# Kernel tuning notes

Measured on AMD Instinct MI355X. Metric: run time of the kernel, lower is better.

The kernel has to match this reference:

```python
import jax, jax.numpy as jnp
import numpy as np

S = 4        # support_num
NEI = 32     # neighbor_num for conv stages
POOL_NEI = 4 # neighbor_num inside Pool_layer
EPS = 1e-12


def sq_dist(a, b):
    # a: (b,m,3), b: (b,n,3) -> (b,m,n)
    return (jnp.sum(a * a, -1)[:, :, None] + jnp.sum(b * b, -1)[:, None, :]
            - 2.0 * jnp.einsum('bmd,bnd->bmn', a, b))


def query_ball(radius, k, points, queries):
    # PointNet++-style ball query: up to k indices within radius, padded with first hit.
    d = sq_dist(queries, points)                      # (b,m,n)
    n = points.shape[1]
    idx = jnp.broadcast_to(jnp.arange(n, dtype=jnp.int32), d.shape)
    idx = jnp.where(d > radius * radius, n, idx)
    idx = jnp.sort(idx, axis=-1)[..., :k]             # (b,m,k)
    first = idx[..., :1]
    return jnp.where(idx == n, first, idx)


def gather_nb(feat, idx):
    # feat: (b,v,c), idx: (b,v,k) -> (b,v,k,c)
    return jax.vmap(lambda f, i: f[i])(feat, idx)


def neighbor_dir_norm(verts, idx):
    nb = gather_nb(verts, idx)                        # (b,v,k,3)
    d = nb - verts[:, :, None, :]
    return d / (jnp.linalg.norm(d, axis=-1, keepdims=True) + EPS)


def conv_surface(idx, verts, dirs):
    # dirs: (3, S*out). Geometric-only first layer of 3DGCN.
    b, v, k = idx.shape
    o = dirs.shape[1] // S
    dn = neighbor_dir_norm(verts, idx)                # (b,v,k,3)
    sd = dirs / (jnp.linalg.norm(dirs, axis=0, keepdims=True) + EPS)
    theta = jnp.maximum(jnp.einsum('bvkd,dm->bvkm', dn, sd), 0.0)
    theta = theta.reshape(b, v, k, S, o)
    return theta.max(axis=2).sum(axis=2)              # (b,v,o)


def conv_layer(idx, verts, feat, w, bias, dirs):
    # w: (cin,(S+1)*o), bias: ((S+1)*o,), dirs: (3,S*o)
    b, v, k = idx.shape
    o = dirs.shape[1] // S
    dn = neighbor_dir_norm(verts, idx)
    sd = dirs / (jnp.linalg.norm(dirs, axis=0, keepdims=True) + EPS)
    theta = jnp.maximum(jnp.einsum('bvkd,dm->bvkm', dn, sd), 0.0)  # (b,v,k,S*o)
    fout = feat @ w + bias                            # (b,v,(S+1)*o)
    center, supp = fout[..., :o], fout[..., o:]
    supp_nb = gather_nb(supp, idx)                    # (b,v,k,S*o)
    act = (theta * supp_nb).reshape(b, v, k, S, o).max(axis=2).sum(axis=2)
    return center + act


def pool(verts, feat, radius):
    idx = query_ball(radius, POOL_NEI, verts, verts)
    pooled = gather_nb(feat, idx).max(axis=2)         # (b,v,c)
    m = verts.shape[1] // 2                           # pooling_rate = 2 (deterministic subsample)
    return verts[:, :m], pooled[:, :m]


def setup_inputs() -> dict:
    key = jax.random.key(0)
    ks = jax.random.split(key, 32)
    B, V = 4, 4096
    inp = {}
    inp['vertices'] = jax.random.uniform(ks[0], (B, V, 3), dtype=jnp.float32)
    inp['surf_dirs'] = jax.random.normal(ks[1], (3, S * 32), dtype=jnp.float32) * 0.1
    specs = [(1, 32, 32), (3, 64, 32), (4, 96, 32), (6, 128, 32), (7, 160, 32),
             (8, 192, 32), (9, 224, 32), (10, 256, 32), (11, 288, 1024)]
    i = 2
    for n, cin, cout in specs:
        inp[f'w{n}'] = jax.random.normal(ks[i], (cin, (S + 1) * cout), dtype=jnp.float32) / np.sqrt(cin); i += 1
        inp[f'b{n}'] = jnp.zeros(((S + 1) * cout,), jnp.float32)
        inp[f'd{n}'] = jax.random.normal(ks[i], (3, S * cout), dtype=jnp.float32) * 0.1; i += 1
    inp['fc1_w'] = jax.random.normal(ks[i], (1024, 256), dtype=jnp.float32) * 0.03; i += 1
    inp['fc1_b'] = jnp.zeros((256,), jnp.float32)
    inp['bn_g'] = jnp.ones((256,), jnp.float32)
    inp['bn_b'] = jnp.zeros((256,), jnp.float32)
    inp['bn_m'] = jnp.zeros((256,), jnp.float32)
    inp['bn_v'] = jnp.ones((256,), jnp.float32)
    inp['fc2_w'] = jax.random.normal(ks[i], (256, 40), dtype=jnp.float32) * 0.06
    inp['fc2_b'] = jnp.zeros((40,), jnp.float32)
    return inp


def reference(vertices, surf_dirs, w1, b1, d1, w3, b3, d3, w4, b4, d4, w6, b6, d6,
              w7, b7, d7, w8, b8, d8, w9, b9, d9, w10, b10, d10, w11, b11, d11,
              fc1_w, fc1_b, bn_g, bn_b, bn_m, bn_v, fc2_w, fc2_b):
    relu = lambda x: jnp.maximum(x, 0.0)
    verts = vertices
    idx = query_ball(0.2, NEI, verts, verts)
    fm0 = relu(conv_surface(idx, verts, surf_dirs))
    fm1 = relu(conv_layer(idx, verts, fm0, w1, b1, d1))
    fm1 = jnp.concatenate([fm0, fm1], -1)
    verts, fm1 = pool(verts, fm1, 0.2)
    idx = query_ball(0.4, NEI, verts, verts)
    fm3 = relu(conv_layer(idx, verts, fm1, w3, b3, d3)); fm3 = jnp.concatenate([fm1, fm3], -1)
    fm4 = relu(conv_layer(idx, verts, fm3, w4, b4, d4)); fm4 = jnp.concatenate([fm3, fm4], -1)
    verts, fm4 = pool(verts, fm4, 0.4)
    idx = query_ball(0.6, NEI, verts, verts)
    fm6 = relu(conv_layer(idx, verts, fm4, w6, b6, d6)); fm6 = jnp.concatenate([fm4, fm6], -1)
    fm7 = relu(conv_layer(idx, verts, fm6, w7, b7, d7)); fm7 = jnp.concatenate([fm6, fm7], -1)
    verts, fm7 = pool(verts, fm7, 0.6)
    idx = query_ball(0.8, NEI, verts, verts)
    fm8 = relu(conv_layer(idx, verts, fm7, w8, b8, d8)); fm8 = jnp.concatenate([fm7, fm8], -1)
    fm9 = relu(conv_layer(idx, verts, fm8, w9, b9, d9)); fm9 = jnp.concatenate([fm8, fm9], -1)
    verts, fm9 = pool(verts, fm9, 0.8)
    idx = query_ball(1.0, NEI, verts, verts)
    fm10 = relu(conv_layer(idx, verts, fm9, w10, b10, d10)); fm10 = jnp.concatenate([fm9, fm10], -1)
    fm11 = conv_layer(idx, verts, fm10, w11, b11, d11)
    g = fm11.max(axis=1)                              # (b,1024) global max pool
    h = g @ fc1_w + fc1_b                             # Dropout is identity at inference
    h = (h - bn_m) / jnp.sqrt(bn_v + 1e-5) * bn_g + bn_b
    h = relu(h)
    return h @ fc2_w + fc2_b                          # (b,40)
```

## Files before the change

kernel.cpp:

```cpp
#include <hip/hip_runtime.h>
#include <hip/hip_bf16.h>
#include <math.h>

#define DEV __device__ __forceinline__

DEV float frn_mul(float a, float b) { return __fmul_rn(a, b); }
DEV float frn_add(float a, float b) { return __fadd_rn(a, b); }

union BFU { __hip_bfloat16 h; unsigned short u; };

typedef __attribute__((ext_vector_type(8))) short short8v;
typedef __attribute__((ext_vector_type(4))) float f32x4;

__global__ void pack4_kernel(const float* __restrict__ v, float4* __restrict__ out,
                             int n)
{
    int t = blockIdx.x * blockDim.x + threadIdx.x;
    if (t >= n) return;
    float x = v[(size_t)t * 3 + 0], y = v[(size_t)t * 3 + 1], z = v[(size_t)t * 3 + 2];
    float pn = frn_add(frn_add(frn_mul(x, x), frn_mul(y, y)), frn_mul(z, z));
    out[t] = make_float4(x, y, z, pn);
}

DEV void qb_scan2(const float4* __restrict__ pts, int V, float4 q4, float r2,
                  int lane, int* __restrict__ row)
{
    float qx = q4.x, qy = q4.y, qz = q4.z, qn = q4.w;
    int count = 0;
    int first = -1;
    float4 pbuf[2];
#pragma unroll
    for (int u = 0; u < 2; ++u) pbuf[u] = pts[u * 64 + lane];
    for (int base = 0; base < V && count < 32; base += 128) {
#pragma unroll
        for (int u = 0; u < 2; ++u) {
            float4 p = pbuf[u];
            pbuf[u] = pts[base + 128 + u * 64 + lane];
            float dt = frn_add(frn_add(frn_mul(qx, p.x), frn_mul(qy, p.y)), frn_mul(qz, p.z));
            float d = __fsub_rn(frn_add(qn, p.w), frn_mul(2.0f, dt));
            bool in = !(d > r2);
            unsigned long long mask = __ballot(in);
            if (first < 0 && mask != 0ull)
                first = base + u * 64 + (int)__ffsll((long long)mask) - 1;
            int pos = count + (int)__popcll(mask & ((1ull << lane) - 1ull));
            if (in && pos < 32) row[pos] = base + u * 64 + lane;
            count += (int)__popcll(mask);
        }
    }
    int cnt = count < 32 ? count : 32;
    for (int t = cnt + lane; t < 32; t += 64) row[t] = first;
}

__global__ __launch_bounds__(256)
void mega_start_kernel(const float4* __restrict__ vp1,
                       const float* __restrict__ dirs,
                       float* __restrict__ outF, int Cw,
                       int* __restrict__ idx1, int* __restrict__ idx2,
                       int* __restrict__ idx3, int* __restrict__ idx4,
                       int* __restrict__ idx5,
                       const float* __restrict__ w11, unsigned short* __restrict__ wt)
{
    __shared__ int rowS[4][32];
    int bid = blockIdx.x;
    int tid = threadIdx.x;
    int lane = tid & 63;

    if (bid < 4096) {
        int wid = (bid * 256 + tid) >> 6;
        int wql = tid >> 6;
        int b = wid >> 12;
        float4 q4 = vp1[(size_t)wid];
        float qx = q4.x, qy = q4.y, qz = q4.z, qn = q4.w;
        const float4* pts = vp1 + (size_t)b * 4096;
        int* row = idx1 + (size_t)wid * 32;

        int count = 0;
        int first = -1;
        float4 pbuf[4];
#pragma unroll
        for (int u = 0; u < 4; ++u) pbuf[u] = pts[u * 64 + lane];
        for (int base = 0; base < 4096 && count < 32; base += 256) {
#pragma unroll
            for (int u = 0; u < 4; ++u) {
                float4 p = pbuf[u];
                pbuf[u] = pts[base + 256 + u * 64 + lane];
                float dt = frn_add(frn_add(frn_mul(qx, p.x), frn_mul(qy, p.y)), frn_mul(qz, p.z));
                float d = __fsub_rn(frn_add(qn, p.w), frn_mul(2.0f, dt));
                bool in = !(d > 0.04f);
                unsigned long long mask = __ballot(in);
                if (first < 0 && mask != 0ull)
                    first = base + u * 64 + (int)__ffsll((long long)mask) - 1;
                int pos = count + (int)__popcll(mask & ((1ull << lane) - 1ull));
                if (in && pos < 32) { row[pos] = base + u * 64 + lane; rowS[wql][pos] = base + u * 64 + lane; }
                count += (int)__popcll(mask);
            }
        }
        int cnt = count < 32 ? count : 32;
        for (int t = cnt + lane; t < 32; t += 64) { row[t] = first; rowS[wql][t] = first; }
        __syncthreads();

        float dnx, dny, dnz;
        {
            int k = lane & 31;
            float4 nb4 = pts[rowS[wql][k]];
            float dx = nb4.x - qx;
            float dy = nb4.y - qy;
            float dz = nb4.z - qz;
            float nrm = sqrtf(dx * dx + dy * dy + dz * dz) + 1e-12f;
            float inv = 1.0f / nrm;
            dnx = dx * inv; dny = dy * inv; dnz = dz * inv;
        }
        int m1 = lane, m2 = lane + 64;
        float ax = dirs[m1], ay = dirs[128 + m1], az = dirs[256 + m1];
        float i1 = 1.0f / (sqrtf(ax * ax + ay * ay + az * az) + 1e-12f);
        ax *= i1; ay *= i1; az *= i1;
        float bx = dirs[m2], by = dirs[128 + m2], bz = dirs[256 + m2];
        float i2 = 1.0f / (sqrtf(bx * bx + by * by + bz * bz) + 1e-12f);
        bx *= i2; by *= i2; bz *= i2;

        float mx1 = -INFINITY, mx2 = -INFINITY;
        for (int k = 0; k < 32; ++k) {
            float ex = __shfl(dnx, k, 64);
            float ey = __shfl(dny, k, 64);
            float ez = __shfl(dnz, k, 64);
            float t1 = fmaxf(ex * ax + ey * ay + ez * az, 0.0f);
            float t2 = fmaxf(ex * bx + ey * by + ez * bz, 0.0f);
            mx1 = fmaxf(mx1, t1);
            mx2 = fmaxf(mx2, t2);
        }
        float part = mx1 + mx2;
        float tot = part + __shfl_xor(part, 32, 64);
        if (lane < 32) {
            outF[(size_t)wid * Cw + lane] = fmaxf(tot, 0.0f);
        }
    } else if (bid < 7936) {
        int V, r_bid; float r2; int* idxp;
        if (bid < 6144)      { V = 2048; r2 = 0.16f; idxp = idx2; r_bid = bid - 4096; }
        else if (bid < 7168) { V = 1024; r2 = 0.36f; idxp = idx3; r_bid = bid - 6144; }
        else if (bid < 7680) { V = 512;  r2 = 0.64f; idxp = idx4; r_bid = bid - 7168; }
        else                 { V = 256;  r2 = 1.0f;  idxp = idx5; r_bid = bid - 7680; }
        int widl = (r_bid * 256 + tid) >> 6;
        int b = widl / V;
        int v = widl - b * V;
        float4 q4 = vp1[(size_t)b * 4096 + v];
        const float4* pts = vp1 + (size_t)b * 4096;
        qb_scan2(pts, V, q4, r2, lane, idxp + (size_t)widl * 32);
    } else {
        int t = (bid - 7936) * 256 + tid;
        if (t < 5120 * 36) {
            int kc = t / 5120;
            int n = t - kc * 5120;
            BFU a;
            ushort4 o0, o1;
            a.h = __float2bfloat16(w11[(size_t)(kc * 8 + 0) * 5120 + n]); o0.x = a.u;
            a.h = __float2bfloat16(w11[(size_t)(kc * 8 + 1) * 5120 + n]); o0.y = a.u;
            a.h = __float2bfloat16(w11[(size_t)(kc * 8 + 2) * 5120 + n]); o0.z = a.u;
            a.h = __float2bfloat16(w11[(size_t)(kc * 8 + 3) * 5120 + n]); o0.w = a.u;
            a.h = __float2bfloat16(w11[(size_t)(kc * 8 + 4) * 5120 + n]); o1.x = a.u;
            a.h = __float2bfloat16(w11[(size_t)(kc * 8 + 5) * 5120 + n]); o1.y = a.u;
            a.h = __float2bfloat16(w11[(size_t)(kc * 8 + 6) * 5120 + n]); o1.z = a.u;
            a.h = __float2bfloat16(w11[(size_t)(kc * 8 + 7) * 5120 + n]); o1.w = a.u;
            *(ushort4*)&wt[(size_t)n * 288 + kc * 8] = o0;
            *(ushort4*)&wt[(size_t)n * 288 + kc * 8 + 4] = o1;
        }
    }
}

__global__ __launch_bounds__(256)
void gemm_tiled_kernel(const float* __restrict__ feat, int Cw, int cin,
                       const float* __restrict__ w, const float* __restrict__ bias,
                       int N, float* __restrict__ fout)
{
    __shared__ float As[64][36];
    __shared__ float Bs[32][68];

    int m0 = blockIdx.x * 64;
    int n0 = blockIdx.y * 64;
    int tid = threadIdx.x;
    int tx = tid & 15, ty = tid >> 4;

    float acc[4][4];
#pragma unroll
    for (int i = 0; i < 4; ++i)
#pragma unroll
        for (int j = 0; j < 4; ++j) acc[i][j] = 0.0f;

    for (int k0 = 0; k0 < cin; k0 += 32) {
#pragma unroll
        for (int i = 0; i < 2; ++i) {
            int qq = tid + i * 256;
            int row = qq >> 3, c = qq & 7;
            float4 v = *(const float4*)&feat[(size_t)(m0 + row) * Cw + k0 + 4 * c];
            *(float4*)&As[row][4 * c] = v;
        }
#pragma unroll
        for (int i = 0; i < 2; ++i) {
            int qq = tid + i * 256;
            int kr = qq >> 4, c = qq & 15;
            int n = n0 + 4 * c;
            float4 v = make_float4(0.0f, 0.0f, 0.0f, 0.0f);
            if (n < N) v = *(const float4*)&w[(size_t)(k0 + kr) * N + n];
            *(float4*)&Bs[kr][4 * c] = v;
        }
        __syncthreads();

#pragma unroll
        for (int kt = 0; kt < 32; kt += 4) {
            float4 av4[4], bv4[4];
#pragma unroll
            for (int i = 0; i < 4; ++i) av4[i] = *(const float4*)&As[ty * 4 + i][kt];
#pragma unroll
            for (int r = 0; r < 4; ++r) bv4[r] = *(const float4*)&Bs[kt + r][tx * 4];
            const float* a = (const float*)av4;
            const float* bb = (const float*)bv4;
#pragma unroll
            for (int i = 0; i < 4; ++i)
#pragma unroll
                for (int r = 0; r < 4; ++r)
#pragma unroll
                    for (int j = 0; j < 4; ++j)
                        acc[i][j] = fmaf(a[i * 4 + r], bb[r * 4 + j], acc[i][j]);
        }
        __syncthreads();
    }

    int n = n0 + tx * 4;
    if (n < N) {
        float b0 = bias[n + 0], b1 = bias[n + 1], b2 = bias[n + 2], b3 = bias[n + 3];
#pragma unroll
        for (int i = 0; i < 4; ++i) {
            int m = m0 + ty * 4 + i;
            float4 o;
            o.x = acc[i][0] + b0;
            o.y = acc[i][1] + b1;
            o.z = acc[i][2] + b2;
            o.w = acc[i][3] + b3;
            *(float4*)&fout[(size_t)m * N + n] = o;
        }
    }
}

__global__ __launch_bounds__(256)
void gemm_mfma_conv11(const unsigned short* __restrict__ Abf,
                      const unsigned short* __restrict__ WTbf,
                      const float* __restrict__ bias,
                      __hip_bfloat16* __restrict__ fout)
{
    __shared__ unsigned short As[128][40];
    __shared__ unsigned short Bs[128][40];
    const int K = 288, N = 5120;
    int m0 = blockIdx.x * 128;
    int n0 = blockIdx.y * 128;
    int tid = threadIdx.x;
    int lane = tid & 63;
    int wave = tid >> 6;
    int wm = wave & 1, wn = wave >> 1;
    int l15 = lane & 15, l4 = lane >> 4;

    f32x4 acc[4][4];
#pragma unroll
    for (int mi = 0; mi < 4; ++mi)
#pragma unroll
        for (int ni = 0; ni < 4; ++ni) acc[mi][ni] = (f32x4){0.f, 0.f, 0.f, 0.f};

    for (int k0 = 0; k0 < K; k0 += 32) {
#pragma unroll
        for (int i = 0; i < 2; ++i) {
            int c = tid + i * 256;
            int row = c >> 2, qq = c & 3;
            *(uint4*)&As[row][qq * 8] = *(const uint4*)&Abf[(size_t)(m0 + row) * K + k0 + qq * 8];
            *(uint4*)&Bs[row][qq * 8] = *(const uint4*)&WTbf[(size_t)(n0 + row) * K + k0 + qq * 8];
        }
        __syncthreads();

        short8v af[4], bfv[4];
#pragma unroll
        for (int mi = 0; mi < 4; ++mi)
            af[mi] = *(const short8v*)&As[wm * 64 + mi * 16 + l15][l4 * 8];
#pragma unroll
        for (int ni = 0; ni < 4; ++ni)
            bfv[ni] = *(const short8v*)&Bs[wn * 64 + ni * 16 + l15][l4 * 8];
#pragma unroll
        for (int mi = 0; mi < 4; ++mi)
#pragma unroll
            for (int ni = 0; ni < 4; ++ni)
                acc[mi][ni] = __builtin_amdgcn_mfma_f32_16x16x32_bf16(af[mi], bfv[ni], acc[mi][ni], 0, 0, 0);
        __syncthreads();
    }

#pragma unroll
    for (int ni = 0; ni < 4; ++ni) {
        int col = n0 + wn * 64 + ni * 16 + l15;
        float bv = bias[col];
#pragma unroll
        for (int mi = 0; mi < 4; ++mi) {
            int rbase = m0 + wm * 64 + mi * 16 + l4 * 4;
#pragma unroll
            for (int j = 0; j < 4; ++j) {
                BFU u;
                u.h = __float2bfloat16(acc[mi][ni][j] + bv);
                *(unsigned short*)&fout[(size_t)(rbase + j) * N + col] = u.u;
            }
        }
    }
}

__global__ void conv_agg32_kernel(const int* __restrict__ idx,
                                  const float4* __restrict__ vp1,
                                  const float* __restrict__ fout,
                                  const float* __restrict__ dirs,
                                  float* __restrict__ outF, int Cw, int coff,
                                  int V, int do_relu,
                                  unsigned short* __restrict__ abf)
{
    int blk = blockIdx.x;
    int b = (blk & 7) >> 1;
    int j = ((blk >> 3) << 1) | (blk & 1);
    int vloc = j * 4 + (int)(threadIdx.x >> 6);
    int wid = b * V + vloc;
    int lane = threadIdx.x & 63;

    float dnx, dny, dnz;
    int nbrow;
    {
        int k = lane & 31;
        int nb = idx[(size_t)wid * 32 + k];
        nbrow = b * V + nb;
        float4 c4 = vp1[(size_t)b * 4096 + vloc];
        float4 n4 = vp1[(size_t)b * 4096 + nb];
        float dx = n4.x - c4.x;
        float dy = n4.y - c4.y;
        float dz = n4.z - c4.z;
        float nrm = sqrtf(dx * dx + dy * dy + dz * dz) + 1e-12f;
        float inv = 1.0f / nrm;
        dnx = dx * inv; dny = dy * inv; dnz = dz * inv;
    }
    int m1 = lane, m2 = lane + 64;
    float ax = dirs[m1], ay = dirs[128 + m1], az = dirs[256 + m1];
    float i1 = 1.0f / (sqrtf(ax * ax + ay * ay + az * az) + 1e-12f);
    ax *= i1; ay *= i1; az *= i1;
    float bx = dirs[m2], by = dirs[128 + m2], bz = dirs[256 + m2];
    float i2 = 1.0f / (sqrtf(bx * bx + by * by + bz * bz) + 1e-12f);
    bx *= i2; by *= i2; bz *= i2;

    float a1[4] = {-INFINITY, -INFINITY, -INFINITY, -INFINITY};
    float a2[4] = {-INFINITY, -INFINITY, -INFINITY, -INFINITY};
#pragma unroll
    for (int kk = 0; kk < 32; kk += 4) {
#pragma unroll
        for (int u = 0; u < 4; ++u) {
            int k = kk + u;
            float ex = __shfl(dnx, k, 64);
            float ey = __shfl(dny, k, 64);
            float ez = __shfl(dnz, k, 64);
            int nr = __shfl(nbrow, k, 64);
            const float* fr = fout + (size_t)nr * 160 + 32;
            float t1 = fmaxf(ex * ax + ey * ay + ez * az, 0.0f);
            float t2 = fmaxf(ex * bx + ey * by + ez * bz, 0.0f);
            a1[u] = fmaxf(a1[u], t1 * fr[m1]);
            a2[u] = fmaxf(a2[u], t2 * fr[m2]);
        }
    }
    float mx1 = fmaxf(fmaxf(a1[0], a1[1]), fmaxf(a1[2], a1[3]));
    float mx2 = fmaxf(fmaxf(a2[0], a2[1]), fmaxf(a2[2], a2[3]));
    float part = mx1 + mx2;
    float tot = part + __shfl_xor(part, 32, 64);
    if (lane < 32) {
        float c = fout[(size_t)wid * 160 + lane];
        float val = c + tot;
        if (do_relu) val = fmaxf(val, 0.0f);
        outF[(size_t)wid * Cw + coff + lane] = val;
        if (abf) {
            BFU u; u.h = __float2bfloat16(val);
            abf[(size_t)wid * 288 + coff + lane] = u.u;
        }
    }
}

__global__ __launch_bounds__(512)
void conv_agg_big_kernel(const int* __restrict__ idx,
                         const float4* __restrict__ vp1,
                         const __hip_bfloat16* __restrict__ fout,
                         const float* __restrict__ dirs,
                         float* __restrict__ G,
                         int V, int B)
{
    __shared__ float dnS[32][3];
    __shared__ long long offS[32];
    __shared__ float sm[512 * 9];
    int blk = blockIdx.x;
    int b = (blk & 7) >> 1;
    int v = ((blk >> 3) << 1) | (blk & 1);
    int row = b * V + v;
    int tid = threadIdx.x;

    if (tid < 32) {
        int nb = idx[(size_t)row * 32 + tid];
        float4 c4 = vp1[(size_t)b * 4096 + v];
        float4 n4 = vp1[(size_t)b * 4096 + nb];
        float dx = n4.x - c4.x;
        float dy = n4.y - c4.y;
        float dz = n4.z - c4.z;
        float nrm = sqrtf(dx * dx + dy * dy + dz * dz) + 1e-12f;
        float inv = 1.0f / nrm;
        dnS[tid][0] = dx * inv; dnS[tid][1] = dy * inv; dnS[tid][2] = dz * inv;
        offS[tid] = (long long)(b * V + nb) * 5120 + 1024;
    }
    __syncthreads();

    int p0 = tid * 8;
    float4 X[2], Y[2], Z[2];
#pragma unroll
    for (int c = 0; c < 2; ++c) {
        X[c] = *(const float4*)&dirs[p0 + 4 * c];
        Y[c] = *(const float4*)&dirs[4096 + p0 + 4 * c];
        Z[c] = *(const float4*)&dirs[8192 + p0 + 4 * c];
    }
    const float* xf = (const float*)X;
    const float* yf = (const float*)Y;
    const float* zf = (const float*)Z;
    float sdx[8], sdy[8], sdz[8], mx[8];
#pragma unroll
    for (int p = 0; p < 8; ++p) {
        float ax = xf[p], ay = yf[p], az = zf[p];
        float inv = 1.0f / (sqrtf(ax * ax + ay * ay + az * az) + 1e-12f);
        sdx[p] = ax * inv; sdy[p] = ay * inv; sdz[p] = az * inv;
        mx[p] = -INFINITY;
    }

#pragma unroll 2
    for (int k = 0; k < 32; ++k) {
        float ex = dnS[k][0], ey = dnS[k][1], ez = dnS[k][2];
        const __hip_bfloat16* fr = fout + offS[k];
        uint4 u0 = *(const uint4*)&fr[p0];
        unsigned int uu[4] = {u0.x, u0.y, u0.z, u0.w};
#pragma unroll
        for (int h = 0; h < 4; ++h) {
            float slo = __uint_as_float(uu[h] << 16);
            float shi = __uint_as_float(uu[h] & 0xFFFF0000u);
            int p = 2 * h;
            float th0 = fmaxf(ex * sdx[p] + ey * sdy[p] + ez * sdz[p], 0.0f);
            float th1 = fmaxf(ex * sdx[p + 1] + ey * sdy[p + 1] + ez * sdz[p + 1], 0.0f);
            mx[p] = fmaxf(mx[p], th0 * slo);
            mx[p + 1] = fmaxf(mx[p + 1], th1 * shi);
        }
    }

#pragma unroll
    for (int p = 0; p < 8; ++p) sm[tid * 9 + p] = mx[p];
    __syncthreads();

#pragma unroll
    for (int q = 0; q < 2; ++q) {
        int oo = q * 512 + tid;
        int t0 = oo >> 3, pp = oo & 7;
        float s0 = sm[t0 * 9 + pp];
        float s1 = sm[(128 + t0) * 9 + pp];
        float s2 = sm[(256 + t0) * 9 + pp];
        float s3 = sm[(384 + t0) * 9 + pp];
        float val = ((s0 + s1) + s2) + s3;
        float c = __bfloat162float(fout[(size_t)row * 5120 + oo]);
        G[(size_t)row * 1024 + oo] = c + val;
    }
}

__global__ void pool_fused_kernel(const int* __restrict__ idx_conv,
                                  int Vp, int Vh, int B,
                                  const float* __restrict__ Fin, int CwIn,
                                  float* __restrict__ Fout, int CwOut, int C,
                                  unsigned short* __restrict__ abf)
{
    int wid = (blockIdx.x * blockDim.x + threadIdx.x) >> 6;
    int lane = threadIdx.x & 63;
    int nq = B * Vh;
    if (wid >= nq) return;
    int b = wid / Vh;
    int v = wid - b * Vh;
    int rowc = b * Vp + v;

    int idv = 0;
    if (lane < 4) idv = idx_conv[(size_t)rowc * 32 + lane];
    int i0 = __shfl(idv, 0, 64);
    int i1 = __shfl(idv, 1, 64);
    int i2 = __shfl(idv, 2, 64);
    int i3 = __shfl(idv, 3, 64);

    const float* r0 = Fin + (size_t)(b * Vp + i0) * CwIn;
    const float* r1 = Fin + (size_t)(b * Vp + i1) * CwIn;
    const float* r2p = Fin + (size_t)(b * Vp + i2) * CwIn;
    const float* r3 = Fin + (size_t)(b * Vp + i3) * CwIn;
    for (int c = lane; c < C; c += 64) {
        float m = fmaxf(fmaxf(r0[c], r1[c]), fmaxf(r2p[c], r3[c]));
        Fout[(size_t)wid * CwOut + c] = m;
        if (abf) {
            BFU u; u.h = __float2bfloat16(m);
            abf[(size_t)wid * 288 + c] = u.u;
        }
    }
}

__global__ void gmax_kernel(const float* __restrict__ G, float* __restrict__ gm,
                            int V)
{
    __shared__ float red[4][64];
    int b = blockIdx.x >> 4;
    int c0 = (blockIdx.x & 15) * 64;
    int t = threadIdx.x;
    int c = c0 + (t & 63);
    int vg = t >> 6;
    float m = -INFINITY;
    for (int v = vg * 64; v < (vg + 1) * 64; ++v)
        m = fmaxf(m, G[((size_t)b * V + v) * 1024 + c]);
    red[vg][t & 63] = m;
    __syncthreads();
    if (t < 64) {
        float r = fmaxf(fmaxf(red[0][t], red[1][t]), fmaxf(red[2][t], red[3][t]));
        gm[b * 1024 + c0 + t] = r;
    }
}

__global__ __launch_bounds__(256)
void fc1_kernel(const float* __restrict__ gm, const float* __restrict__ w1,
                const float* __restrict__ b1_,
                const float* __restrict__ bn_g, const float* __restrict__ bn_b,
                const float* __restrict__ bn_m, const float* __restrict__ bn_v,
                float* __restrict__ h)
{
    __shared__ float gs[1024];
    __shared__ float red[8][32];
    int b = blockIdx.y;
    int j0 = blockIdx.x * 32;
    int t = threadIdx.x;
    for (int i = t; i < 1024; i += 256) gs[i] = gm[b * 1024 + i];
    __syncthreads();
    int jj = t & 31, kk = t >> 5;
    int j = j0 + jj;
    const float* wp = w1 + (size_t)(kk * 128) * 256 + j;
    float acc = 0.0f;
#pragma unroll 8
    for (int k = 0; k < 128; ++k)
        acc = fmaf(gs[kk * 128 + k], wp[(size_t)k * 256], acc);
    red[kk][jj] = acc;
    __syncthreads();
    if (t < 32) {
        float s = 0.0f;
#pragma unroll
        for (int q = 0; q < 8; ++q) s += red[q][t];
        int jw = j0 + t;
        s += b1_[jw];
        s = (s - bn_m[jw]) / sqrtf(bn_v[jw] + 1e-5f) * bn_g[jw] + bn_b[jw];
        h[b * 256 + jw] = fmaxf(s, 0.0f);
    }
}

__global__ void fc2_kernel(const float* __restrict__ h, const float* __restrict__ w2,
                           const float* __restrict__ b2_, float* __restrict__ out)
{
    __shared__ float hs[256];
    int b = blockIdx.x;
    int t = threadIdx.x;
    hs[t] = h[b * 256 + t];
    __syncthreads();
    if (t < 40) {
        float acc = 0.0f;
#pragma unroll 8
        for (int k = 0; k < 256; ++k) acc = fmaf(hs[k], w2[(size_t)k * 40 + t], acc);
        out[b * 40 + t] = acc + b2_[t];
    }
}

static inline int wblocks(int waves) { return (waves + 3) / 4; }
static inline int tblocks(int threads) { return (threads + 255) / 256; }
static inline dim3 ggrid(int M, int N) { return dim3(M / 64, (N + 63) / 64); }

extern "C" void kernel_launch(void* const* d_in, const int* in_sizes, int n_in,
                              void* d_out, int out_size, void* d_ws, size_t ws_size,
                              hipStream_t stream)
{
    const int B = 4;
    const float* verts1 = (const float*)d_in[0];
    const float* surf_dirs = (const float*)d_in[1];
    const float* w1 = (const float*)d_in[2];
    const float* b1 = (const float*)d_in[3];
    const float* d1 = (const float*)d_in[4];
    const float* w3 = (const float*)d_in[5];
    const float* b3 = (const float*)d_in[6];
    const float* d3 = (const float*)d_in[7];
    const float* w4 = (const float*)d_in[8];
    const float* b4 = (const float*)d_in[9];
    const float* d4 = (const float*)d_in[10];
    const float* w6 = (const float*)d_in[11];
    const float* b6 = (const float*)d_in[12];
    const float* d6 = (const float*)d_in[13];
    const float* w7 = (const float*)d_in[14];
    const float* b7 = (const float*)d_in[15];
    const float* d7 = (const float*)d_in[16];
    const float* w8 = (const float*)d_in[17];
    const float* b8 = (const float*)d_in[18];
    const float* d8 = (const float*)d_in[19];
    const float* w9 = (const float*)d_in[20];
    const float* b9 = (const float*)d_in[21];
    const float* d9 = (const float*)d_in[22];
    const float* w10 = (const float*)d_in[23];
    const float* b10 = (const float*)d_in[24];
    const float* d10 = (const float*)d_in[25];
    const float* w11 = (const float*)d_in[26];
    const float* b11 = (const float*)d_in[27];
    const float* d11 = (const float*)d_in[28];
    const float* fc1_w = (const float*)d_in[29];
    const float* fc1_b = (const float*)d_in[30];
    const float* bn_g = (const float*)d_in[31];
    const float* bn_b = (const float*)d_in[32];
    const float* bn_m = (const float*)d_in[33];
    const float* bn_v = (const float*)d_in[34];
    const float* fc2_w = (const float*)d_in[35];
    const float* fc2_b = (const float*)d_in[36];
    (void)in_sizes; (void)n_in; (void)out_size; (void)ws_size;

    float* ws = (float*)d_ws;
    size_t off = 0;
    auto alloc = [&](size_t n) { float* p = ws + off; off += n; return p; };
    float* fout = alloc(4 * 256 * 5120);
    int* idx1 = (int*)alloc(4 * 4096 * 32);
    int* idx2 = (int*)alloc(4 * 2048 * 32);
    int* idx3 = (int*)alloc(4 * 1024 * 32);
    int* idx4 = (int*)alloc(4 * 512 * 32);
    int* idx5 = (int*)alloc(4 * 256 * 32);
    float* F1 = alloc(4 * 4096 * 64);
    float* L2 = alloc(4 * 2048 * 128);
    float* L3 = alloc(4 * 1024 * 192);
    float* L4 = alloc(4 * 512 * 256);
    float* L5 = alloc(4 * 256 * 288);
    float* G = alloc(4 * 256 * 1024);
    float4* vp1 = (float4*)alloc((4 * 4096 + 512) * 4);
    float* gm = alloc(4 * 1024);
    float* hh = alloc(4 * 256);

    unsigned short* Abf = (unsigned short*)G;
    unsigned short* WTbf = Abf + 1024 * 288;

    pack4_kernel<<<tblocks(B * 4096), 256, 0, stream>>>(verts1, vp1, B * 4096);
    mega_start_kernel<<<8656, 256, 0, stream>>>(vp1, surf_dirs, F1, 64,
                                                idx1, idx2, idx3, idx4, idx5,
                                                w11, WTbf);

    gemm_tiled_kernel<<<ggrid(B * 4096, 160), 256, 0, stream>>>(F1, 64, 32, w1, b1, 160, fout);
    conv_agg32_kernel<<<B * 4096 / 4, 256, 0, stream>>>(idx1, vp1, fout, d1, F1, 64, 32, 4096, 1, nullptr);
    pool_fused_kernel<<<wblocks(B * 2048), 256, 0, stream>>>(idx1, 4096, 2048, B, F1, 64, L2, 128, 64, nullptr);

    gemm_tiled_kernel<<<ggrid(B * 2048, 160), 256, 0, stream>>>(L2, 128, 64, w3, b3, 160, fout);
    conv_agg32_kernel<<<B * 2048 / 4, 256, 0, stream>>>(idx2, vp1, fout, d3, L2, 128, 64, 2048, 1, nullptr);
    gemm_tiled_kernel<<<ggrid(B * 2048, 160), 256, 0, stream>>>(L2, 128, 96, w4, b4, 160, fout);
    conv_agg32_kernel<<<B * 2048 / 4, 256, 0, stream>>>(idx2, vp1, fout, d4, L2, 128, 96, 2048, 1, nullptr);
    pool_fused_kernel<<<wblocks(B * 1024), 256, 0, stream>>>(idx2, 2048, 1024, B, L2, 128, L3, 192, 128, nullptr);

    gemm_tiled_kernel<<<ggrid(B * 1024, 160), 256, 0, stream>>>(L3, 192, 128, w6, b6, 160, fout);
    conv_agg32_kernel<<<B * 1024 / 4, 256, 0, stream>>>(idx3, vp1, fout, d6, L3, 192, 128, 1024, 1, nullptr);
    gemm_tiled_kernel<<<ggrid(B * 1024, 160), 256, 0, stream>>>(L3, 192, 160, w7, b7, 160, fout);
    conv_agg32_kernel<<<B * 1024 / 4, 256, 0, stream>>>(idx3, vp1, fout, d7, L3, 192, 160, 1024, 1, nullptr);
    pool_fused_kernel<<<wblocks(B * 512), 256, 0, stream>>>(idx3, 1024, 512, B, L3, 192, L4, 256, 192, nullptr);

    gemm_tiled_kernel<<<ggrid(B * 512, 160), 256, 0, stream>>>(L4, 256, 192, w8, b8, 160, fout);
    conv_agg32_kernel<<<B * 512 / 4, 256, 0, stream>>>(idx4, vp1, fout, d8, L4, 256, 192, 512, 1, nullptr);
    gemm_tiled_kernel<<<ggrid(B * 512, 160), 256, 0, stream>>>(L4, 256, 224, w9, b9, 160, fout);
    conv_agg32_kernel<<<B * 512 / 4, 256, 0, stream>>>(idx4, vp1, fout, d9, L4, 256, 224, 512, 1, nullptr);
    pool_fused_kernel<<<wblocks(B * 256), 256, 0, stream>>>(idx4, 512, 256, B, L4, 256, L5, 288, 256, Abf);

    gemm_tiled_kernel<<<ggrid(B * 256, 160), 256, 0, stream>>>(L5, 288, 256, w10, b10, 160, fout);
    conv_agg32_kernel<<<B * 256 / 4, 256, 0, stream>>>(idx5, vp1, fout, d10, L5, 288, 256, 256, 1, Abf);
    __hip_bfloat16* fout_bf = (__hip_bfloat16*)fout;
    gemm_mfma_conv11<<<dim3(8, 40), 256, 0, stream>>>(Abf, WTbf, b11, fout_bf);
    conv_agg_big_kernel<<<B * 256, 512, 0, stream>>>(idx5, vp1, fout_bf, d11, G, 256, B);

    gmax_kernel<<<64, 256, 0, stream>>>(G, gm, 256);
    fc1_kernel<<<dim3(8, B), 256, 0, stream>>>(gm, fc1_w, fc1_b, bn_g, bn_b, bn_m, bn_v, hh);
    fc2_kernel<<<B, 256, 0, stream>>>(hh, fc2_w, fc2_b, (float*)d_out);
}
```

Baseline: 414.0 us.

## Assign one block per query in first-stage ball query and surface conv

The first-level ball query plus surface convolution now uses a whole 256-thread block per query point instead of one wave per query. The four waves scan 256 points per step, combine their ballot masks through shared memory to compute output positions, and split the 128 directions between two waves, reducing through shared memory. This shortens the serial scan chain per query and spreads the work over many more blocks, at the cost of a block-wide barrier every iteration and two idle waves during the direction stage.

Result: slower. 442.2 us (+6.8%).

```diff
diff --git a/kernel.cpp b/kernel.cpp
--- a/kernel.cpp
+++ b/kernel.cpp
@@ -60,85 +60,96 @@
                        int* __restrict__ idx5,
                        const float* __restrict__ w11, unsigned short* __restrict__ wt)
 {
-    __shared__ int rowS[4][32];
+    __shared__ unsigned long long maskL[2][4];
+    __shared__ int rowS[32];
+    __shared__ float MS[128];
     int bid = blockIdx.x;
     int tid = threadIdx.x;
     int lane = tid & 63;
 
-    if (bid < 4096) {
-        int wid = (bid * 256 + tid) >> 6;
-        int wql = tid >> 6;
+    if (bid < 16384) {
+        int wid = bid;
         int b = wid >> 12;
+        int wave = tid >> 6;
         float4 q4 = vp1[(size_t)wid];
         float qx = q4.x, qy = q4.y, qz = q4.z, qn = q4.w;
         const float4* pts = vp1 + (size_t)b * 4096;
         int* row = idx1 + (size_t)wid * 32;
+        unsigned long long lmask = (1ull << lane) - 1ull;
 
         int count = 0;
         int first = -1;
-        float4 pbuf[4];
-#pragma unroll
-        for (int u = 0; u < 4; ++u) pbuf[u] = pts[u * 64 + lane];
-        for (int base = 0; base < 4096 && count < 32; base += 256) {
-#pragma unroll
-            for (int u = 0; u < 4; ++u) {
-                float4 p = pbuf[u];
-                pbuf[u] = pts[base + 256 + u * 64 + lane];
-                float dt = frn_add(frn_add(frn_mul(qx, p.x), frn_mul(qy, p.y)), frn_mul(qz, p.z));
-                float d = __fsub_rn(frn_add(qn, p.w), frn_mul(2.0f, dt));
-                bool in = !(d > 0.04f);
-                unsigned long long mask = __ballot(in);
-                if (first < 0 && mask != 0ull)
-                    first = base + u * 64 + (int)__ffsll((long long)mask) - 1;
-                int pos = count + (int)__popcll(mask & ((1ull << lane) - 1ull));
-                if (in && pos < 32) { row[pos] = base + u * 64 + lane; rowS[wql][pos] = base + u * 64 + lane; }
-                count += (int)__popcll(mask);
+        int ib = 0;
+        float4 p = pts[wave * 64 + lane];
+        for (int base = 0; base < 4096 && count < 32; base += 256, ib ^= 1) {
+            float4 pnx = pts[base + 256 + wave * 64 + lane];
+            float dt = frn_add(frn_add(frn_mul(qx, p.x), frn_mul(qy, p.y)), frn_mul(qz, p.z));
+            float d = __fsub_rn(frn_add(qn, p.w), frn_mul(2.0f, dt));
+            bool in = !(d > 0.04f);
+            unsigned long long mask = __ballot(in);
+            if (lane == 0) maskL[ib][wave] = mask;
+            __syncthreads();
+            unsigned long long m0 = maskL[ib][0], m1 = maskL[ib][1];
+            unsigned long long m2 = maskL[ib][2], m3 = maskL[ib][3];
+            int c0 = (int)__popcll(m0), c1 = (int)__popcll(m1);
+            int c2 = (int)__popcll(m2), c3 = (int)__popcll(m3);
+            if (first < 0) {
+                if (m0) first = base + (int)__ffsll((long long)m0) - 1;
+                else if (m1) first = base + 64 + (int)__ffsll((long long)m1) - 1;
+                else if (m2) first = base + 128 + (int)__ffsll((long long)m2) - 1;
+                else if (m3) first = base + 192 + (int)__ffsll((long long)m3) - 1;
             }
+            int off = count;
+            if (wave > 0) off += c0;
+            if (wave > 1) off += c1;
+            if (wave > 2) off += c2;
+            int pos = off + (int)__popcll(mask & lmask);
+            if (in && pos < 32) {
+                int vv = base + wave * 64 + lane;
+                row[pos] = vv; rowS[pos] = vv;
+            }
+            count += c0 + c1 + c2 + c3;
+            p = pnx;
         }
         int cnt = count < 32 ? count : 32;
-        for (int t = cnt + lane; t < 32; t += 64) { row[t] = first; rowS[wql][t] = first; }
+        for (int t = cnt + tid; t < 32; t += 256) { row[t] = first; rowS[t] = first; }
         __syncthreads();
 
-        float dnx, dny, dnz;
-        {
+        if (wave < 2) {
             int k = lane & 31;
-            float4 nb4 = pts[rowS[wql][k]];
+            float4 nb4 = pts[rowS[k]];
             float dx = nb4.x - qx;
             float dy = nb4.y - qy;
             float dz = nb4.z - qz;
             float nrm = sqrtf(dx * dx + dy * dy + dz * dz) + 1e-12f;
             float inv = 1.0f / nrm;
-            dnx = dx * inv; dny = dy * inv; dnz = dz * inv;
-        }
-        int m1 = lane, m2 = lane + 64;
-        float ax = dirs[m1], ay = dirs[128 + m1], az = dirs[256 + m1];
-        float i1 = 1.0f / (sqrtf(ax * ax + ay * ay + az * az) + 1e-12f);
-        ax *= i1; ay *= i1; az *= i1;
-        float bx = dirs[m2], by = dirs[128 + m2], bz = dirs[256 + m2];
-        float i2 = 1.0f / (sqrtf(bx * bx + by * by + bz * bz) + 1e-12f);
-        bx *= i2; by *= i2; bz *= i2;
-
-        float mx1 = -INFINITY, mx2 = -INFINITY;
-        for (int k = 0; k < 32; ++k) {
-            float ex = __shfl(dnx, k, 64);
-            float ey = __shfl(dny, k, 64);
-            float ez = __shfl(dnz, k, 64);
-            float t1 = fmaxf(ex * ax + ey * ay + ez * az, 0.0f);
-            float t2 = fmaxf(ex * bx + ey * by + ez * bz, 0.0f);
-            mx1 = fmaxf(mx1, t1);
-            mx2 = fmaxf(mx2, t2);
-        }
-        float part = mx1 + mx2;
-        float tot = part + __shfl_xor(part, 32, 64);
-        if (lane < 32) {
-            outF[(size_t)wid * Cw + lane] = fmaxf(tot, 0.0f);
-        }
-    } else if (bid < 7936) {
+            float dnx = dx * inv, dny = dy * inv, dnz = dz * inv;
+            int m = wave * 64 + lane;
+            float ax = dirs[m], ay = dirs[128 + m], az = dirs[256 + m];
+            float i1 = 1.0f / (sqrtf(ax * ax + ay * ay + az * az) + 1e-12f);
+            ax *= i1; ay *= i1; az *= i1;
+            float mx = -INFINITY;
+            for (int k2 = 0; k2 < 32; ++k2) {
+                float ex = __shfl(dnx, k2, 64);
+                float ey = __shfl(dny, k2, 64);
+                float ez = __shfl(dnz, k2, 64);
+                float t1 = fmaxf(ex * ax + ey * ay + ez * az, 0.0f);
+                mx = fmaxf(mx, t1);
+            }
+            MS[m] = mx;
+        }
+        __syncthreads();
+        if (tid < 32) {
+            float s0 = MS[tid] + MS[tid + 64];
+            float s1 = MS[tid + 32] + MS[tid + 96];
+            outF[(size_t)wid * Cw + tid] = fmaxf(s0 + s1, 0.0f);
+        }
+    } else if (bid < 20224) {
         int V, r_bid; float r2; int* idxp;
-        if (bid < 6144)      { V = 2048; r2 = 0.16f; idxp = idx2; r_bid = bid - 4096; }
-        else if (bid < 7168) { V = 1024; r2 = 0.36f; idxp = idx3; r_bid = bid - 6144; }
-        else if (bid < 7680) { V = 512;  r2 = 0.64f; idxp = idx4; r_bid = bid - 7168; }
-        else                 { V = 256;  r2 = 1.0f;  idxp = idx5; r_bid = bid - 7680; }
+        if (bid < 18432)      { V = 2048; r2 = 0.16f; idxp = idx2; r_bid = bid - 16384; }
+        else if (bid < 19456) { V = 1024; r2 = 0.36f; idxp = idx3; r_bid = bid - 18432; }
+        else if (bid < 19968) { V = 512;  r2 = 0.64f; idxp = idx4; r_bid = bid - 19456; }
+        else                  { V = 256;  r2 = 1.0f;  idxp = idx5; r_bid = bid - 19968; }
         int widl = (r_bid * 256 + tid) >> 6;
         int b = widl / V;
         int v = widl - b * V;
@@ -146,7 +157,7 @@
         const float4* pts = vp1 + (size_t)b * 4096;
         qb_scan2(pts, V, q4, r2, lane, idxp + (size_t)widl * 32);
     } else {
-        int t = (bid - 7936) * 256 + tid;
+        int t = (bid - 20224) * 256 + tid;
         if (t < 5120 * 36) {
             int kc = t / 5120;
             int n = t - kc * 5120;
@@ -640,9 +651,9 @@
     unsigned short* WTbf = Abf + 1024 * 288;
 
     pack4_kernel<<<tblocks(B * 4096), 256, 0, stream>>>(verts1, vp1, B * 4096);
-    mega_start_kernel<<<8656, 256, 0, stream>>>(vp1, surf_dirs, F1, 64,
-                                                idx1, idx2, idx3, idx4, idx5,
-                                                w11, WTbf);
+    mega_start_kernel<<<20944, 256, 0, stream>>>(vp1, surf_dirs, F1, 64,
+                                                 idx1, idx2, idx3, idx4, idx5,
+                                                 w11, WTbf);
 
     gemm_tiled_kernel<<<ggrid(B * 4096, 160), 256, 0, stream>>>(F1, 64, 32, w1, b1, 160, fout);
     conv_agg32_kernel<<<B * 4096 / 4, 256, 0, stream>>>(idx1, vp1, fout, d1, F1, 64, 32, 4096, 1, nullptr);
```
